# Kernel tuning notes

Measured on AMD Instinct MI355X. Metric: run time of the kernel, lower is better.

## Reference

```python
import jax, jax.numpy as jnp
import numpy as np

DIM = 768
HEADS = 12
DIM_HEAD = DIM // HEADS
FACTOR = DIM_HEAD ** (-0.5)
B, T = 4, 2048


def setup_inputs() -> dict:
    key = jax.random.key(0)
    k1, k2, k3 = jax.random.split(key, 3)
    x = jax.random.normal(k1, (B, T, DIM), dtype=jnp.float32)
    # VarianceScaling-like init scale for linear weights
    W_qkv = jax.random.normal(k2, (DIM, 3 * DIM), dtype=jnp.float32) * (DIM ** -0.5)
    W_out = jax.random.normal(k3, (DIM, DIM), dtype=jnp.float32) * (DIM ** -0.5)
    return {"x": x, "W_qkv": W_qkv, "W_out": W_out}


def reference(x, W_qkv, W_out):
    b, t, _ = x.shape
    qkv = x @ W_qkv  # [b, t, 3*dim]
    # einops 'b t (d k h) -> k b h t d' with k=3, h=HEADS: d slowest, k middle, h fastest
    qkv = qkv.reshape(b, t, DIM_HEAD, 3, HEADS)
    qkv = jnp.transpose(qkv, (3, 0, 4, 1, 2))  # [3, b, h, t, d]
    q, k, v = qkv[0], qkv[1], qkv[2]
    # scaled dot-product attention, full [b,h,t,t] scores as in the original
    scores = jnp.einsum('bhid,bhjd->bhij', q, k) * FACTOR
    attn = jax.nn.softmax(scores, axis=-1)
    out = jnp.einsum('bhij,bhjd->bhid', attn, v)  # [b, h, t, d]
    # 'b h t d -> b t (h d)'
    out = jnp.transpose(out, (0, 2, 1, 3)).reshape(b, t, HEADS * DIM_HEAD)
    return out @ W_out
```

## Files before the change

### kernel.cpp

```cpp
#include <hip/hip_runtime.h>
#include <hip/hip_bf16.h>

#define DIM    768
#define HEADS  12
#define DHEAD  64
#define BATCH  4
#define SEQ    2048
#define NROW   (BATCH * SEQ)
#define QKVN   (3 * DIM)
#define FACTOR 0.125f
#define QSCALE 0.18033688011112042f

typedef __attribute__((ext_vector_type(8))) short short8;
typedef __attribute__((ext_vector_type(4))) float floatx4;
typedef __attribute__((ext_vector_type(16))) float floatx16;
typedef __attribute__((ext_vector_type(4))) unsigned uintx4;

__device__ __forceinline__ floatx4 mfma16(short8 a, short8 b, floatx4 c) {
    return __builtin_amdgcn_mfma_f32_16x16x32_bf16(a, b, c, 0, 0, 0);
}
__device__ __forceinline__ floatx16 mfma32(short8 a, short8 b, floatx16 c) {
    return __builtin_amdgcn_mfma_f32_32x32x16_bf16(a, b, c, 0, 0, 0);
}

__device__ __forceinline__ void glds16(const void* g, void* l) {
    __builtin_amdgcn_global_load_lds((const __attribute__((address_space(1))) void*)g,
                                     (__attribute__((address_space(3))) void*)l,
                                     16, 0, 0);
}

__device__ __forceinline__ short rne16(float f) {
    unsigned u = __builtin_bit_cast(unsigned, f);
    return (short)((u + 0x7fffu + ((u >> 16) & 1u)) >> 16);
}
__device__ __forceinline__ unsigned pack2(float lo, float hi) {
    unsigned ul = __builtin_bit_cast(unsigned, lo);
    unsigned uh = __builtin_bit_cast(unsigned, hi);
    ul = (ul + 0x7fffu + ((ul >> 16) & 1u)) >> 16;
    uh = (uh + 0x7fffu + ((uh >> 16) & 1u)) & 0xffff0000u;
    return ul | uh;
}
__device__ __forceinline__ unsigned cvtpk(float lo, float hi) {
    unsigned r;
    asm("v_cvt_pk_bf16_f32 %0, %1, %2" : "=v"(r) : "v"(lo), "v"(hi));
    return r;
}

__device__ __forceinline__ int swz8(int row, int col) {
    return (row << 6) + ((((col >> 3) ^ row) & 7) << 3) + (col & 7);
}

__global__ __launch_bounds__(256) void prep(const float* __restrict__ x,
                                            short* __restrict__ xb,
                                            const float* __restrict__ Wqkv,
                                            short* __restrict__ Wqt,
                                            const float* __restrict__ Wout,
                                            short* __restrict__ Wot) {
    __shared__ short T[32][33];
    int blk = blockIdx.x;
    if (blk < 6144) {
        int g = blk * 256 + threadIdx.x;
        float4 v = ((const float4*)x)[g];
        uint2 o;
        o.x = pack2(v.x, v.y);
        o.y = pack2(v.z, v.w);
        ((uint2*)xb)[g] = o;
        return;
    }
    blk -= 6144;
    const float* W;
    short* Wt;
    int N, permute, bx, by;
    if (blk < 1728) { W = Wqkv; Wt = Wqt; N = QKVN; permute = 1; bx = blk % 72; by = blk / 72; }
    else { blk -= 1728; W = Wout; Wt = Wot; N = DIM; permute = 0; bx = blk % 24; by = blk / 24; }

    int n0 = bx * 32, k0 = by * 32;
    int c = threadIdx.x & 31, r0 = threadIdx.x >> 5;
    for (int r = r0; r < 32; r += 8)
        T[r][c] = rne16(W[(size_t)(k0 + r) * N + n0 + c]);
    __syncthreads();
    for (int r = r0; r < 32; r += 8) {
        int n = n0 + r;
        int np = n;
        float scale = 1.0f;
        if (permute) {
            int d = n / 36, rem = n - d * 36;
            int which = rem / 12, h = rem - which * 12;
            np = which * 768 + h * 64 + d;
            if (which == 0) scale = QSCALE;
        }
        float v = __bfloat162float(__hip_bfloat16_raw{(unsigned short)T[c][r]});
        Wt[(size_t)np * DIM + k0 + c] = (scale == 1.0f) ? T[c][r] : rne16(v * scale);
    }
}

__global__ __launch_bounds__(256) void gemm_qkv(const short* __restrict__ A,
                                                const short* __restrict__ Bt,
                                                short* __restrict__ Qo,
                                                short* __restrict__ Ko,
                                                short* __restrict__ Vto) {
    __shared__ short As[128 * 64];
    __shared__ short Bs[128 * 64];
    const int tid = threadIdx.x;
    const int lane = tid & 63, wave = tid >> 6;
    const int l15 = lane & 15, quad = lane >> 4;

    const int flat = blockIdx.x;
    const int xcd = flat & 7;
    const int local = flat >> 3;
    const int mloc = local & 7, nloc = local >> 3;
    const int m0 = (xcd * 8 + mloc) * 128;
    const int n0 = nloc * 128;

    const int wm = (wave >> 1) * 64, wn = (wave & 1) * 64;
    const int r8 = wave * 8 + (lane >> 3);
    const int c8 = lane & 7;
    const int sc = ((c8 ^ (r8 & 7)) << 3);

    const int sn = n0 + wn;
    const int which = sn / 768;
    const bool swapAB = (which != 2);

    floatx4 acc[4][4] = {};
    for (int k0 = 0; k0 < DIM; k0 += 64) {
#pragma unroll
        for (int i = 0; i < 4; ++i) {
            int row = i * 32 + r8;
            glds16(&A[(size_t)(m0 + row) * DIM + k0 + sc], &As[(size_t)(i * 32 + wave * 8) * 64]);
            glds16(&Bt[(size_t)(n0 + row) * DIM + k0 + sc], &Bs[(size_t)(i * 32 + wave * 8) * 64]);
        }
        __syncthreads();
#pragma unroll
        for (int ks = 0; ks < 2; ++ks) {
            short8 a[4], b[4];
#pragma unroll
            for (int mt = 0; mt < 4; ++mt)
                a[mt] = *(const short8*)&As[swz8(wm + mt * 16 + l15, ks * 32 + quad * 8)];
#pragma unroll
            for (int nt = 0; nt < 4; ++nt)
                b[nt] = *(const short8*)&Bs[swz8(wn + nt * 16 + l15, ks * 32 + quad * 8)];
            if (swapAB) {
#pragma unroll
                for (int mt = 0; mt < 4; ++mt)
#pragma unroll
                    for (int nt = 0; nt < 4; ++nt)
                        acc[mt][nt] = mfma16(b[nt], a[mt], acc[mt][nt]);
            } else {
#pragma unroll
                for (int mt = 0; mt < 4; ++mt)
#pragma unroll
                    for (int nt = 0; nt < 4; ++nt)
                        acc[mt][nt] = mfma16(a[mt], b[nt], acc[mt][nt]);
            }
        }
        __syncthreads();
    }

    const int h = (sn - which * 768) >> 6;
    const int bb = (m0 + wm) >> 11;

    if (which != 2) {
        const bool isQ = (which == 0);
        short* dst = isQ ? Qo : Ko;
        const size_t tb = isQ
            ? ((size_t)(bb * HEADS + h) * 16 + ((m0 & 2047) >> 7)) * 8192
            : ((size_t)(bb * HEADS + h) * 32 + (((m0 + wm) & 2047) >> 6)) * 4096;
#pragma unroll
        for (int mt = 0; mt < 4; ++mt)
#pragma unroll
            for (int nt = 0; nt < 4; ++nt) {
                int cl = (mt & 1) * 16 + l15 + 32 * (quad >> 1);
                int off = isQ
                    ? (((wm >> 5) + (mt >> 1)) * 2048 + nt * 512 + cl * 8 + (quad & 1) * 4)
                    : (((mt >> 1) * 4 + nt) * 512 + cl * 8 + (quad & 1) * 4);
                uint2 pk;
                pk.x = pack2(acc[mt][nt][0], acc[mt][nt][1]);
                pk.y = pack2(acc[mt][nt][2], acc[mt][nt][3]);
                *(uint2*)&dst[tb + off] = pk;
            }
    } else {
        const size_t tb = ((size_t)(bb * HEADS + h) * 32 + (((m0 + wm) & 2047) >> 6)) * 4096;
#pragma unroll
        for (int mt = 0; mt < 4; ++mt)
#pragma unroll
            for (int nt = 0; nt < 4; ++nt) {
                int cl = (nt & 1) * 16 + l15 + 32 * (quad >> 1);
                int off = ((nt >> 1) * 4 + mt) * 512 + cl * 8 + (quad & 1) * 4;
                uint2 pk;
                pk.x = pack2(acc[mt][nt][0], acc[mt][nt][1]);
                pk.y = pack2(acc[mt][nt][2], acc[mt][nt][3]);
                *(uint2*)&Vto[tb + off] = pk;
            }
    }
}

__global__ __launch_bounds__(256, 3) void attn_mfma(const short* __restrict__ Q,
                                                    const short* __restrict__ K,
                                                    const short* __restrict__ Vt,
                                                    short* __restrict__ O) {
    __shared__ __align__(16) short smem[24576];
    const int tid = threadIdx.x;
    const int lane = tid & 63, wave = tid >> 6;
    const int l31 = lane & 31, hi = lane >> 5;
    const int flat = blockIdx.x;
    const int xcd = flat & 7, li = flat >> 3;
    const int bh = xcd + (li % 6) * 8;
    const int q0 = (li / 6) * 128;
    const size_t base = (size_t)bh * SEQ * DHEAD;
    const int lane8 = lane * 8;

    {
        size_t qtb = base + (size_t)(q0 >> 7) * 8192;
#pragma unroll
        for (int c = 0; c < 4; ++c) {
            int s = wave * 4 + c;
            glds16(&Q[qtb + s * 512 + lane8], &smem[s * 512]);
        }
    }
    __syncthreads();
    short8 qf[4];
#pragma unroll
    for (int ks = 0; ks < 4; ++ks)
        qf[ks] = *(const short8*)&smem[wave * 2048 + ks * 512 + lane8];
    __syncthreads();

    floatx16 o0 = {}, o1 = {};
    float lsum = 0.f;

    const int seg0 = (2 * wave + 0) * 512;
    const int seg1 = (2 * wave + 1) * 512;

#define STAGE(tt, buf) {                                                \
        size_t ktb_ = base + (size_t)(tt) * 4096;                       \
        glds16(&K[ktb_ + seg0 + lane8], &(buf)[seg0]);                  \
        glds16(&K[ktb_ + seg1 + lane8], &(buf)[seg1]);                  \
        glds16(&Vt[ktb_ + seg0 + lane8], &(buf)[4096 + seg0]);          \
        glds16(&Vt[ktb_ + seg1 + lane8], &(buf)[4096 + seg1]);          \
    }

#define SOFTPACK(SA, PFA, PFB) {                                              \
        float e0_  = __builtin_amdgcn_exp2f(SA[0]);                           \
        float e1_  = __builtin_amdgcn_exp2f(SA[1]);                           \
        float e2_  = __builtin_amdgcn_exp2f(SA[2]);                           \
        float e3_  = __builtin_amdgcn_exp2f(SA[3]);                           \
        float e4_  = __builtin_amdgcn_exp2f(SA[4]);                           \
        float e5_  = __builtin_amdgcn_exp2f(SA[5]);                           \
        float e6_  = __builtin_amdgcn_exp2f(SA[6]);                           \
        float e7_  = __builtin_amdgcn_exp2f(SA[7]);                           \
        float e8_  = __builtin_amdgcn_exp2f(SA[8]);                           \
        float e9_  = __builtin_amdgcn_exp2f(SA[9]);                           \
        float e10_ = __builtin_amdgcn_exp2f(SA[10]);                          \
        float e11_ = __builtin_amdgcn_exp2f(SA[11]);                          \
        float e12_ = __builtin_amdgcn_exp2f(SA[12]);                          \
        float e13_ = __builtin_amdgcn_exp2f(SA[13]);                          \
        float e14_ = __builtin_amdgcn_exp2f(SA[14]);                          \
        float e15_ = __builtin_amdgcn_exp2f(SA[15]);                          \
        lsum += (((e0_ + e1_) + (e2_ + e3_)) + ((e4_ + e5_) + (e6_ + e7_)))   \
              + (((e8_ + e9_) + (e10_ + e11_)) + ((e12_ + e13_) + (e14_ + e15_))); \
        unsigned A0_ = cvtpk(e0_, e1_),   A1_ = cvtpk(e2_, e3_);              \
        unsigned B0_ = cvtpk(e4_, e5_),   B1_ = cvtpk(e6_, e7_);              \
        unsigned C0_ = cvtpk(e8_, e9_),   C1_ = cvtpk(e10_, e11_);            \
        unsigned E0_ = cvtpk(e12_, e13_), E1_ = cvtpk(e14_, e15_);            \
        asm("v_permlane32_swap_b32 %0, %1" : "+v"(A0_), "+v"(B0_));           \
        asm("v_permlane32_swap_b32 %0, %1" : "+v"(A1_), "+v"(B1_));           \
        asm("v_permlane32_swap_b32 %0, %1" : "+v"(C0_), "+v"(E0_));           \
        asm("v_permlane32_swap_b32 %0, %1" : "+v"(C1_), "+v"(E1_));           \
        uintx4 wa_ = {A0_, A1_, B0_, B1_};                                    \
        uintx4 wb_ = {C0_, C1_, E0_, E1_};                                    \
        PFA = __builtin_bit_cast(short8, wa_);                                \
        PFB = __builtin_bit_cast(short8, wb_);                                \
    }

    short8 pfp[4];

    STAGE(0, smem);
    {
        __syncthreads();
        STAGE(1, smem + 8192);
        floatx16 sa0 = {}, sa1 = {};
        __builtin_amdgcn_s_setprio(1);
#pragma unroll
        for (int c = 0; c < 4; ++c) {
            short8 kf0 = *(const short8*)&smem[c * 512 + lane8];
            short8 kf1 = *(const short8*)&smem[(4 + c) * 512 + lane8];
            sa0 = mfma32(kf0, qf[c], sa0);
            sa1 = mfma32(kf1, qf[c], sa1);
        }
        __builtin_amdgcn_s_setprio(0);
        SOFTPACK(sa0, pfp[0], pfp[1])
        SOFTPACK(sa1, pfp[2], pfp[3])
    }

    int bp = 0, bc = 1, bn = 2;
    for (int t = 1; t < 32; ++t) {
        __syncthreads();
        const short* curb = smem + bc * 8192;
        const short* prvv = smem + bp * 8192 + 4096;
        if (t < 31)
            STAGE(t + 1, smem + bn * 8192);

        floatx16 sa0 = {}, sa1 = {};
        __builtin_amdgcn_s_setprio(1);
#pragma unroll
        for (int c = 0; c < 4; ++c) {
            short8 kf0 = *(const short8*)&curb[c * 512 + lane8];
            short8 kf1 = *(const short8*)&curb[(4 + c) * 512 + lane8];
            short8 vf0 = *(const short8*)&prvv[c * 512 + lane8];
            short8 vf1 = *(const short8*)&prvv[(4 + c) * 512 + lane8];
            sa0 = mfma32(kf0, qf[c], sa0);
            o0  = mfma32(vf0, pfp[c], o0);
            sa1 = mfma32(kf1, qf[c], sa1);
            o1  = mfma32(vf1, pfp[c], o1);
        }
        __builtin_amdgcn_s_setprio(0);

        SOFTPACK(sa0, pfp[0], pfp[1])
        SOFTPACK(sa1, pfp[2], pfp[3])

        bp = bc; bc = bn; bn = (bn == 2) ? 0 : bn + 1;
    }
    {
        const short* prvv = smem + bp * 8192 + 4096;
        __builtin_amdgcn_s_setprio(1);
#pragma unroll
        for (int c = 0; c < 4; ++c) {
            short8 vf0 = *(const short8*)&prvv[c * 512 + lane8];
            short8 vf1 = *(const short8*)&prvv[(4 + c) * 512 + lane8];
            o0 = mfma32(vf0, pfp[c], o0);
            o1 = mfma32(vf1, pfp[c], o1);
        }
        __builtin_amdgcn_s_setprio(0);
    }

#undef SOFTPACK
#undef STAGE

    float s = lsum + __shfl_xor(lsum, 32);
    float inv = 1.f / s;

    const int b = bh / HEADS, h = bh - b * HEADS;
    const int tq = q0 + wave * 32 + l31;
    size_t rowo = ((size_t)(b * SEQ + tq)) * DIM + h * DHEAD;
#pragma unroll
    for (int blk = 0; blk < 4; ++blk) {
        int d0 = 8 * blk + 4 * hi;
        uint2 p0, p1;
        p0.x = cvtpk(o0[4 * blk + 0] * inv, o0[4 * blk + 1] * inv);
        p0.y = cvtpk(o0[4 * blk + 2] * inv, o0[4 * blk + 3] * inv);
        *(uint2*)&O[rowo + d0] = p0;
        p1.x = cvtpk(o1[4 * blk + 0] * inv, o1[4 * blk + 1] * inv);
        p1.y = cvtpk(o1[4 * blk + 2] * inv, o1[4 * blk + 3] * inv);
        *(uint2*)&O[rowo + 32 + d0] = p1;
    }
}

__global__ __launch_bounds__(256) void gemm_out(const short* __restrict__ A,
                                                const short* __restrict__ Bt,
                                                float* __restrict__ out) {
    __shared__ short As[64 * 64];
    __shared__ short Bs[128 * 64];
    const int tid = threadIdx.x;
    const int lane = tid & 63, wave = tid >> 6;
    const int l15 = lane & 15, quad = lane >> 4;
    const int m0 = blockIdx.y * 64, n0 = blockIdx.x * 128;
    const int wn = wave * 32;
    const int r8 = wave * 8 + (lane >> 3);
    const int sc = (((lane & 7) ^ (r8 & 7)) << 3);

    floatx4 acc[4][2] = {};
    for (int k0 = 0; k0 < DIM; k0 += 64) {
#pragma unroll
        for (int i = 0; i < 2; ++i) {
            int row = i * 32 + r8;
            glds16(&A[(size_t)(m0 + row) * DIM + k0 + sc], &As[(size_t)(i * 32 + wave * 8) * 64]);
        }
#pragma unroll
        for (int i = 0; i < 4; ++i) {
            int row = i * 32 + r8;
            glds16(&Bt[(size_t)(n0 + row) * DIM + k0 + sc], &Bs[(size_t)(i * 32 + wave * 8) * 64]);
        }
        __syncthreads();
#pragma unroll
        for (int ks = 0; ks < 2; ++ks) {
            short8 a[4], b[2];
#pragma unroll
            for (int mt = 0; mt < 4; ++mt)
                a[mt] = *(const short8*)&As[swz8(mt * 16 + l15, ks * 32 + quad * 8)];
#pragma unroll
            for (int nt = 0; nt < 2; ++nt)
                b[nt] = *(const short8*)&Bs[swz8(wn + nt * 16 + l15, ks * 32 + quad * 8)];
#pragma unroll
            for (int mt = 0; mt < 4; ++mt)
#pragma unroll
                for (int nt = 0; nt < 2; ++nt)
                    acc[mt][nt] = mfma16(b[nt], a[mt], acc[mt][nt]);
        }
        __syncthreads();
    }

#pragma unroll
    for (int mt = 0; mt < 4; ++mt)
#pragma unroll
        for (int nt = 0; nt < 2; ++nt) {
            int m = m0 + mt * 16 + l15;
            int n = n0 + wn + nt * 16 + quad * 4;
            *(floatx4*)&out[(size_t)m * DIM + n] = acc[mt][nt];
        }
}

extern "C" void kernel_launch(void* const* d_in, const int* in_sizes, int n_in,
                              void* d_out, int out_size, void* d_ws, size_t ws_size,
                              hipStream_t stream) {
    const float* x    = (const float*)d_in[0];
    const float* Wqkv = (const float*)d_in[1];
    const float* Wout = (const float*)d_in[2];
    float* out = (float*)d_out;

    const size_t NE = (size_t)NROW * DIM;
    short* xb  = (short*)d_ws;
    short* Wqt = xb + NE;
    short* Wot = Wqt + (size_t)QKVN * DIM;
    short* Qw  = Wot + (size_t)DIM * DIM;
    short* Kw  = Qw + NE;
    short* Vtw = Kw + NE;

    prep<<<6144 + 1728 + 576, 256, 0, stream>>>(x, xb, Wqkv, Wqt, Wout, Wot);
    gemm_qkv<<<8 * 8 * 18, 256, 0, stream>>>(xb, Wqt, Qw, Kw, Vtw);
    attn_mfma<<<768, 256, 0, stream>>>(Qw, Kw, Vtw, xb);
    gemm_out<<<dim3(DIM / 128, NROW / 64), 256, 0, stream>>>(xb, Wot, out);
}
```

Baseline: 206.1 us.

## Double attention query tile per block to reuse K/V loads across two row groups

Each attention block now handles 256 query rows instead of 128, so every wave computes two 32-row groups against the same staged K and V tiles. The grid halves to 384 blocks and launch bounds drop to two blocks per SIMD to make room for the doubled accumulators. This is meant to halve K/V global and LDS traffic per query and give more independent MFMA work between barriers. The cost is higher register pressure, lower occupancy and fewer blocks than CUs (384 on 256 CUs), which can leave the tail unbalanced.

```diff
diff --git a/kernel.cpp b/kernel.cpp
--- a/kernel.cpp
+++ b/kernel.cpp
@@ -194,7 +194,7 @@
     }
 }
 
-__global__ __launch_bounds__(256, 3) void attn_mfma(const short* __restrict__ Q,
+__global__ __launch_bounds__(256, 2) void attn_mfma(const short* __restrict__ Q,
                                                     const short* __restrict__ K,
                                                     const short* __restrict__ Vt,
                                                     short* __restrict__ O) {
@@ -205,27 +205,29 @@
     const int flat = blockIdx.x;
     const int xcd = flat & 7, li = flat >> 3;
     const int bh = xcd + (li % 6) * 8;
-    const int q0 = (li / 6) * 128;
+    const int q0 = (li / 6) * 256;
     const size_t base = (size_t)bh * SEQ * DHEAD;
     const int lane8 = lane * 8;
 
     {
         size_t qtb = base + (size_t)(q0 >> 7) * 8192;
 #pragma unroll
-        for (int c = 0; c < 4; ++c) {
-            int s = wave * 4 + c;
+        for (int c = 0; c < 8; ++c) {
+            int s = wave * 8 + c;
             glds16(&Q[qtb + s * 512 + lane8], &smem[s * 512]);
         }
     }
     __syncthreads();
-    short8 qf[4];
-#pragma unroll
-    for (int ks = 0; ks < 4; ++ks)
-        qf[ks] = *(const short8*)&smem[wave * 2048 + ks * 512 + lane8];
+    short8 qf[2][4];
+#pragma unroll
+    for (int g = 0; g < 2; ++g)
+#pragma unroll
+        for (int ks = 0; ks < 4; ++ks)
+            qf[g][ks] = *(const short8*)&smem[(wave * 2 + g) * 2048 + ks * 512 + lane8];
     __syncthreads();
 
-    floatx16 o0 = {}, o1 = {};
-    float lsum = 0.f;
+    floatx16 o00 = {}, o01 = {}, o10 = {}, o11 = {};
+    float ls0 = 0.f, ls1 = 0.f;
 
     const int seg0 = (2 * wave + 0) * 512;
     const int seg1 = (2 * wave + 1) * 512;
@@ -238,7 +240,7 @@
         glds16(&Vt[ktb_ + seg1 + lane8], &(buf)[4096 + seg1]);          \
     }
 
-#define SOFTPACK(SA, PFA, PFB) {                                              \
+#define SOFTPACK(SA, PFA, PFB, LS) {                                          \
         float e0_  = __builtin_amdgcn_exp2f(SA[0]);                           \
         float e1_  = __builtin_amdgcn_exp2f(SA[1]);                           \
         float e2_  = __builtin_amdgcn_exp2f(SA[2]);                           \
@@ -255,8 +257,8 @@
         float e13_ = __builtin_amdgcn_exp2f(SA[13]);                          \
         float e14_ = __builtin_amdgcn_exp2f(SA[14]);                          \
         float e15_ = __builtin_amdgcn_exp2f(SA[15]);                          \
-        lsum += (((e0_ + e1_) + (e2_ + e3_)) + ((e4_ + e5_) + (e6_ + e7_)))   \
-              + (((e8_ + e9_) + (e10_ + e11_)) + ((e12_ + e13_) + (e14_ + e15_))); \
+        LS += (((e0_ + e1_) + (e2_ + e3_)) + ((e4_ + e5_) + (e6_ + e7_)))     \
+            + (((e8_ + e9_) + (e10_ + e11_)) + ((e12_ + e13_) + (e14_ + e15_))); \
         unsigned A0_ = cvtpk(e0_, e1_),   A1_ = cvtpk(e2_, e3_);              \
         unsigned B0_ = cvtpk(e4_, e5_),   B1_ = cvtpk(e6_, e7_);              \
         unsigned C0_ = cvtpk(e8_, e9_),   C1_ = cvtpk(e10_, e11_);            \
@@ -271,24 +273,28 @@
         PFB = __builtin_bit_cast(short8, wb_);                                \
     }
 
-    short8 pfp[4];
+    short8 pfp[2][4];
 
     STAGE(0, smem);
     {
         __syncthreads();
         STAGE(1, smem + 8192);
-        floatx16 sa0 = {}, sa1 = {};
+        floatx16 sa00 = {}, sa01 = {}, sa10 = {}, sa11 = {};
         __builtin_amdgcn_s_setprio(1);
 #pragma unroll
         for (int c = 0; c < 4; ++c) {
             short8 kf0 = *(const short8*)&smem[c * 512 + lane8];
             short8 kf1 = *(const short8*)&smem[(4 + c) * 512 + lane8];
-            sa0 = mfma32(kf0, qf[c], sa0);
-            sa1 = mfma32(kf1, qf[c], sa1);
+            sa00 = mfma32(kf0, qf[0][c], sa00);
+            sa10 = mfma32(kf0, qf[1][c], sa10);
+            sa01 = mfma32(kf1, qf[0][c], sa01);
+            sa11 = mfma32(kf1, qf[1][c], sa11);
         }
         __builtin_amdgcn_s_setprio(0);
-        SOFTPACK(sa0, pfp[0], pfp[1])
-        SOFTPACK(sa1, pfp[2], pfp[3])
+        SOFTPACK(sa00, pfp[0][0], pfp[0][1], ls0)
+        SOFTPACK(sa01, pfp[0][2], pfp[0][3], ls0)
+        SOFTPACK(sa10, pfp[1][0], pfp[1][1], ls1)
+        SOFTPACK(sa11, pfp[1][2], pfp[1][3], ls1)
     }
 
     int bp = 0, bc = 1, bn = 2;
@@ -299,7 +305,7 @@
         if (t < 31)
             STAGE(t + 1, smem + bn * 8192);
 
-        floatx16 sa0 = {}, sa1 = {};
+        floatx16 sa00 = {}, sa01 = {}, sa10 = {}, sa11 = {};
         __builtin_amdgcn_s_setprio(1);
 #pragma unroll
         for (int c = 0; c < 4; ++c) {
@@ -307,15 +313,21 @@
             short8 kf1 = *(const short8*)&curb[(4 + c) * 512 + lane8];
             short8 vf0 = *(const short8*)&prvv[c * 512 + lane8];
             short8 vf1 = *(const short8*)&prvv[(4 + c) * 512 + lane8];
-            sa0 = mfma32(kf0, qf[c], sa0);
-            o0  = mfma32(vf0, pfp[c], o0);
-            sa1 = mfma32(kf1, qf[c], sa1);
-            o1  = mfma32(vf1, pfp[c], o1);
+            sa00 = mfma32(kf0, qf[0][c], sa00);
+            o00  = mfma32(vf0, pfp[0][c], o00);
+            sa10 = mfma32(kf0, qf[1][c], sa10);
+            o10  = mfma32(vf0, pfp[1][c], o10);
+            sa01 = mfma32(kf1, qf[0][c], sa01);
+            o01  = mfma32(vf1, pfp[0][c], o01);
+            sa11 = mfma32(kf1, qf[1][c], sa11);
+            o11  = mfma32(vf1, pfp[1][c], o11);
         }
         __builtin_amdgcn_s_setprio(0);
 
-        SOFTPACK(sa0, pfp[0], pfp[1])
-        SOFTPACK(sa1, pfp[2], pfp[3])
+        SOFTPACK(sa00, pfp[0][0], pfp[0][1], ls0)
+        SOFTPACK(sa01, pfp[0][2], pfp[0][3], ls0)
+        SOFTPACK(sa10, pfp[1][0], pfp[1][1], ls1)
+        SOFTPACK(sa11, pfp[1][2], pfp[1][3], ls1)
 
         bp = bc; bc = bn; bn = (bn == 2) ? 0 : bn + 1;
     }
@@ -326,8 +338,10 @@
         for (int c = 0; c < 4; ++c) {
             short8 vf0 = *(const short8*)&prvv[c * 512 + lane8];
             short8 vf1 = *(const short8*)&prvv[(4 + c) * 512 + lane8];
-            o0 = mfma32(vf0, pfp[c], o0);
-            o1 = mfma32(vf1, pfp[c], o1);
+            o00 = mfma32(vf0, pfp[0][c], o00);
+            o10 = mfma32(vf0, pfp[1][c], o10);
+            o01 = mfma32(vf1, pfp[0][c], o01);
+            o11 = mfma32(vf1, pfp[1][c], o11);
         }
         __builtin_amdgcn_s_setprio(0);
     }
@@ -335,22 +349,41 @@
 #undef SOFTPACK
 #undef STAGE
 
-    float s = lsum + __shfl_xor(lsum, 32);
-    float inv = 1.f / s;
+    float s0 = ls0 + __shfl_xor(ls0, 32);
+    float s1 = ls1 + __shfl_xor(ls1, 32);
+    float inv0 = 1.f / s0;
+    float inv1 = 1.f / s1;
 
     const int b = bh / HEADS, h = bh - b * HEADS;
-    const int tq = q0 + wave * 32 + l31;
-    size_t rowo = ((size_t)(b * SEQ + tq)) * DIM + h * DHEAD;
-#pragma unroll
-    for (int blk = 0; blk < 4; ++blk) {
-        int d0 = 8 * blk + 4 * hi;
-        uint2 p0, p1;
-        p0.x = cvtpk(o0[4 * blk + 0] * inv, o0[4 * blk + 1] * inv);
-        p0.y = cvtpk(o0[4 * blk + 2] * inv, o0[4 * blk + 3] * inv);
-        *(uint2*)&O[rowo + d0] = p0;
-        p1.x = cvtpk(o1[4 * blk + 0] * inv, o1[4 * blk + 1] * inv);
-        p1.y = cvtpk(o1[4 * blk + 2] * inv, o1[4 * blk + 3] * inv);
-        *(uint2*)&O[rowo + 32 + d0] = p1;
+    {
+        int tq = q0 + wave * 64 + l31;
+        size_t rowo = ((size_t)(b * SEQ + tq)) * DIM + h * DHEAD;
+#pragma unroll
+        for (int blk = 0; blk < 4; ++blk) {
+            int d0 = 8 * blk + 4 * hi;
+            uint2 p0, p1;
+            p0.x = cvtpk(o00[4 * blk + 0] * inv0, o00[4 * blk + 1] * inv0);
+            p0.y = cvtpk(o00[4 * blk + 2] * inv0, o00[4 * blk + 3] * inv0);
+            *(uint2*)&O[rowo + d0] = p0;
+            p1.x = cvtpk(o01[4 * blk + 0] * inv0, o01[4 * blk + 1] * inv0);
+            p1.y = cvtpk(o01[4 * blk + 2] * inv0, o01[4 * blk + 3] * inv0);
+            *(uint2*)&O[rowo + 32 + d0] = p1;
+        }
+    }
+    {
+        int tq = q0 + wave * 64 + 32 + l31;
+        size_t rowo = ((size_t)(b * SEQ + tq)) * DIM + h * DHEAD;
+#pragma unroll
+        for (int blk = 0; blk < 4; ++blk) {
+            int d0 = 8 * blk + 4 * hi;
+            uint2 p0, p1;
+            p0.x = cvtpk(o10[4 * blk + 0] * inv1, o10[4 * blk + 1] * inv1);
+            p0.y = cvtpk(o10[4 * blk + 2] * inv1, o10[4 * blk + 3] * inv1);
+            *(uint2*)&O[rowo + d0] = p0;
+            p1.x = cvtpk(o11[4 * blk + 0] * inv1, o11[4 * blk + 1] * inv1);
+            p1.y = cvtpk(o11[4 * blk + 2] * inv1, o11[4 * blk + 3] * inv1);
+            *(uint2*)&O[rowo + 32 + d0] = p1;
+        }
     }
 }
 
@@ -426,6 +459,6 @@
 
     prep<<<6144 + 1728 + 576, 256, 0, stream>>>(x, xb, Wqkv, Wqt, Wout, Wot);
     gemm_qkv<<<8 * 8 * 18, 256, 0, stream>>>(xb, Wqt, Qw, Kw, Vtw);
-    attn_mfma<<<768, 256, 0, stream>>>(Qw, Kw, Vtw, xb);
+    attn_mfma<<<384, 256, 0, stream>>>(Qw, Kw, Vtw, xb);
     gemm_out<<<dim3(DIM / 128, NROW / 64), 256, 0, stream>>>(xb, Wot, out);
 }
```

Measured after the change: 212.0 us. 1.03x slower.

## Double-buffer QKV GEMM LDS tiles with K-step 32 prefetch

Applied to the files above, without the earlier changes.

Moves the QKV projection GEMM from single-buffered 64-wide K tiles, which needed two barriers per step, to double-buffered 32-wide K tiles. The next tile's global-to-LDS load is issued before the MFMAs on the current tile, and each step needs only one barrier. The LDS swizzle is changed to match 32-column rows. This adds more loop iterations with fewer MFMAs between barriers, which may limit how much latency the overlap can hide.

```diff
diff --git a/kernel.cpp b/kernel.cpp
--- a/kernel.cpp
+++ b/kernel.cpp
@@ -99,8 +99,8 @@
                                                 short* __restrict__ Qo,
                                                 short* __restrict__ Ko,
                                                 short* __restrict__ Vto) {
-    __shared__ short As[128 * 64];
-    __shared__ short Bs[128 * 64];
+    __shared__ short As[2][4096];
+    __shared__ short Bs[2][4096];
     const int tid = threadIdx.x;
     const int lane = tid & 63, wave = tid >> 6;
     const int l15 = lane & 15, quad = lane >> 4;
@@ -113,48 +113,60 @@
     const int n0 = nloc * 128;
 
     const int wm = (wave >> 1) * 64, wn = (wave & 1) * 64;
-    const int r8 = wave * 8 + (lane >> 3);
-    const int c8 = lane & 7;
-    const int sc = ((c8 ^ (r8 & 7)) << 3);
+
+    const int rl = lane >> 2;
+    const int sch = ((lane & 3) ^ (rl & 3)) << 3;
+    const int s0 = wave * 2, s1 = wave * 2 + 1;
+    const size_t arow0 = (size_t)(m0 + s0 * 16 + rl) * DIM + sch;
+    const size_t arow1 = (size_t)(m0 + s1 * 16 + rl) * DIM + sch;
+    const size_t brow0 = (size_t)(n0 + s0 * 16 + rl) * DIM + sch;
+    const size_t brow1 = (size_t)(n0 + s1 * 16 + rl) * DIM + sch;
 
     const int sn = n0 + wn;
     const int which = sn / 768;
     const bool swapAB = (which != 2);
 
     floatx4 acc[4][4] = {};
-    for (int k0 = 0; k0 < DIM; k0 += 64) {
-#pragma unroll
-        for (int i = 0; i < 4; ++i) {
-            int row = i * 32 + r8;
-            glds16(&A[(size_t)(m0 + row) * DIM + k0 + sc], &As[(size_t)(i * 32 + wave * 8) * 64]);
-            glds16(&Bt[(size_t)(n0 + row) * DIM + k0 + sc], &Bs[(size_t)(i * 32 + wave * 8) * 64]);
-        }
+
+#define STG(koff, bf) {                                          \
+        glds16(&A[arow0 + (koff)], &As[bf][s0 * 512]);           \
+        glds16(&A[arow1 + (koff)], &As[bf][s1 * 512]);           \
+        glds16(&Bt[brow0 + (koff)], &Bs[bf][s0 * 512]);          \
+        glds16(&Bt[brow1 + (koff)], &Bs[bf][s1 * 512]);          \
+    }
+
+    STG(0, 0)
+    for (int t = 0; t < 24; ++t) {
         __syncthreads();
-#pragma unroll
-        for (int ks = 0; ks < 2; ++ks) {
-            short8 a[4], b[4];
+        if (t < 23) STG((t + 1) * 32, (t + 1) & 1)
+        const short* as = As[t & 1];
+        const short* bs = Bs[t & 1];
+        short8 a[4], b[4];
+#pragma unroll
+        for (int mt = 0; mt < 4; ++mt) {
+            int row = wm + mt * 16 + l15;
+            a[mt] = *(const short8*)&as[row * 32 + ((quad ^ (row & 3)) << 3)];
+        }
+#pragma unroll
+        for (int nt = 0; nt < 4; ++nt) {
+            int row = wn + nt * 16 + l15;
+            b[nt] = *(const short8*)&bs[row * 32 + ((quad ^ (row & 3)) << 3)];
+        }
+        if (swapAB) {
 #pragma unroll
             for (int mt = 0; mt < 4; ++mt)
-                a[mt] = *(const short8*)&As[swz8(wm + mt * 16 + l15, ks * 32 + quad * 8)];
-#pragma unroll
-            for (int nt = 0; nt < 4; ++nt)
-                b[nt] = *(const short8*)&Bs[swz8(wn + nt * 16 + l15, ks * 32 + quad * 8)];
-            if (swapAB) {
-#pragma unroll
-                for (int mt = 0; mt < 4; ++mt)
-#pragma unroll
-                    for (int nt = 0; nt < 4; ++nt)
-                        acc[mt][nt] = mfma16(b[nt], a[mt], acc[mt][nt]);
-            } else {
-#pragma unroll
-                for (int mt = 0; mt < 4; ++mt)
-#pragma unroll
-                    for (int nt = 0; nt < 4; ++nt)
-                        acc[mt][nt] = mfma16(a[mt], b[nt], acc[mt][nt]);
-            }
-        }
-        __syncthreads();
-    }
+#pragma unroll
+                for (int nt = 0; nt < 4; ++nt)
+                    acc[mt][nt] = mfma16(b[nt], a[mt], acc[mt][nt]);
+        } else {
+#pragma unroll
+            for (int mt = 0; mt < 4; ++mt)
+#pragma unroll
+                for (int nt = 0; nt < 4; ++nt)
+                    acc[mt][nt] = mfma16(a[mt], b[nt], acc[mt][nt]);
+        }
+    }
+#undef STG
 
     const int h = (sn - which * 768) >> 6;
     const int bb = (m0 + wm) >> 11;
```

New measurement: 213.1 us. +3.4%, slower.
